# Performance work log

Measured on AMD Instinct MI355X. Metric: run time of the kernel, lower is better.

The kernel has to match this reference:

```python
import jax, jax.numpy as jnp
import numpy as np
from jax import lax


def _b3_kernel_2d(dtype=jnp.float32):
    k1 = jnp.array([1.0 / 16.0, 1.0 / 4.0, 3.0 / 8.0, 1.0 / 4.0, 1.0 / 16.0], dtype=dtype)
    return jnp.outer(k1, k1)  # (5, 5)


def _dilated_b3_conv(x, kernel_2d, dilation):
    # PyTorch Conv2d(kernel_size=5, dilation=d, padding=2*d, padding_mode='reflect')
    pad = 2 * dilation
    xp = jnp.pad(x, ((0, 0), (0, 0), (pad, pad), (pad, pad)), mode='reflect')
    k = kernel_2d[None, None, :, :]  # (O=1, I=1, 5, 5)
    return lax.conv_general_dilated(
        xp, k,
        window_strides=(1, 1),
        padding='VALID',
        rhs_dilation=(dilation, dilation),
        dimension_numbers=('NCHW', 'OIHW', 'NCHW'),
    )


def setup_inputs() -> dict:
    key = jax.random.key(0)
    B, H, W = 16, 1024, 1024
    x = jax.random.normal(key, (B, 1, H, W), dtype=jnp.float32)
    kernel_2d = _b3_kernel_2d(jnp.float32)
    return {"x": x, "kernel_2d": kernel_2d, "n_scales": 5}


def reference(x, kernel_2d, n_scales):
    # a trous starlet transform: detail_j = c_j - c_{j+1}; last channel = coarse
    detail_scales = []
    coarse = x
    for scale_idx in range(n_scales - 1):
        dilation = 2 ** scale_idx
        next_coarse = _dilated_b3_conv(coarse, kernel_2d, dilation)
        detail_scales.append(coarse - next_coarse)
        coarse = next_coarse
    all_scales = detail_scales + [coarse]
    return jnp.concatenate(all_scales, axis=1)  # (B, n_scales, H, W)
```

## Files before the change

### kernel.cpp

```cpp
#include <hip/hip_runtime.h>

#define TX 64
#define TY 64

template<int D>
__global__ __launch_bounds__(256)
void starlet_scale(const float* __restrict__ in, long in_bs,
                   float* __restrict__ det,      long det_bs,
                   float* __restrict__ coa,      long coa_bs)
{
    constexpr int H = 1024, W = 1024;
    constexpr int R  = 2 * D;
    constexpr int LW = TX + 2 * R;
    constexpr int LH = TY + 2 * R;
    constexpr int LS = LW + 1;

    __shared__ float tile[LH * LS];
    __shared__ float htmp[LH * TX];

    const int tid = threadIdx.x;
    const int bx  = blockIdx.x * TX;
    const int by  = blockIdx.y * TY;
    const int b   = blockIdx.z;

    const float* __restrict__ inp = in + (long)b * in_bs;

    const float k0 = 0.0625f;
    const float k1 = 0.25f;
    const float k2 = 0.375f;

    for (int i = tid; i < LH * LW; i += 256) {
        int ly = i / LW;
        int lx = i - ly * LW;
        int gy = by - R + ly;
        gy = (gy < 0) ? -gy : ((gy >= H) ? (2 * H - 2 - gy) : gy);
        int gx = bx - R + lx;
        gx = (gx < 0) ? -gx : ((gx >= W) ? (2 * W - 2 - gx) : gx);
        tile[ly * LS + lx] = inp[(long)gy * W + gx];
    }
    __syncthreads();

    for (int i = tid; i < LH * TX; i += 256) {
        int r = i >> 6;
        int x = i & (TX - 1);
        const float* t = &tile[r * LS + x];
        htmp[i] = k0 * (t[0] + t[4 * D]) + k1 * (t[D] + t[3 * D]) + k2 * t[2 * D];
    }
    __syncthreads();

    for (int i = tid; i < TY * TX; i += 256) {
        int y = i >> 6;
        int x = i & (TX - 1);
        const float* h = &htmp[y * TX + x];
        float conv = k0 * (h[0] + h[4 * D * TX])
                   + k1 * (h[D * TX] + h[3 * D * TX])
                   + k2 * h[2 * D * TX];
        float center = tile[(y + R) * LS + (x + R)];
        long gidx = (long)(by + y) * W + (bx + x);
        det[(long)b * det_bs + gidx] = center - conv;
        coa[(long)b * coa_bs + gidx] = conv;
    }
}

extern "C" void kernel_launch(void* const* d_in, const int* in_sizes, int n_in,
                              void* d_out, int out_size, void* d_ws, size_t ws_size,
                              hipStream_t stream) {
    const float* x = (const float*)d_in[0];
    float* out = (float*)d_out;
    float* ws  = (float*)d_ws;

    const long HW = 1024L * 1024L;
    const long OB = 5 * HW;

    dim3 grid(1024 / TX, 1024 / TY, 16);
    dim3 block(256);

    starlet_scale<1><<<grid, block, 0, stream>>>(x, HW, out + 0 * HW, OB, ws, HW);
    starlet_scale<2><<<grid, block, 0, stream>>>(ws, HW, out + 1 * HW, OB, out + 4 * HW, OB);
    starlet_scale<4><<<grid, block, 0, stream>>>(out + 4 * HW, OB, out + 2 * HW, OB, ws, HW);
    starlet_scale<8><<<grid, block, 0, stream>>>(ws, HW, out + 3 * HW, OB, out + 4 * HW, OB);
}
```

Baseline: 513.2 us.

## Fuse starlet scales pairwise into two kernels with float4 tiles and WG swizzle

```diff
diff --git a/kernel.cpp b/kernel.cpp
--- a/kernel.cpp
+++ b/kernel.cpp
@@ -1,64 +1,238 @@
 #include <hip/hip_runtime.h>
 
-#define TX 64
-#define TY 64
-
-template<int D>
-__global__ __launch_bounds__(256)
-void starlet_scale(const float* __restrict__ in, long in_bs,
-                   float* __restrict__ det,      long det_bs,
-                   float* __restrict__ coa,      long coa_bs)
+
+constexpr int H = 1024, W = 1024;
+constexpr long HW = (long)H * W;
+constexpr long OB = 5 * HW;
+constexpr int NT = 256;
+
+__device__ __forceinline__ int reflect_i(int g, int n) {
+    g = (g < 0) ? -g : g;
+    return (g >= n) ? (2 * n - 2 - g) : g;
+}
+
+__device__ __forceinline__ void swizzle_wg(int gx, int gy, int& tx, int& ty, int& tb) {
+    const int nwg = gx * gy * (int)gridDim.z;
+    const int lin = (int)blockIdx.x + gx * ((int)blockIdx.y + gy * (int)blockIdx.z);
+    const int work = (lin & 7) * (nwg >> 3) + (lin >> 3);
+    tx = work % gx;
+    const int rest = work / gx;
+    ty = rest % gy;
+    tb = rest / gy;
+}
+
+__device__ __forceinline__ float4 f4sub(float4 a, float4 b) {
+    return float4{a.x - b.x, a.y - b.y, a.z - b.z, a.w - b.w};
+}
+
+__global__ __launch_bounds__(256, 3)
+void starlet_s01(const float* __restrict__ in, float* __restrict__ out, float* __restrict__ ws)
 {
-    constexpr int H = 1024, W = 1024;
-    constexpr int R  = 2 * D;
-    constexpr int LW = TX + 2 * R;
-    constexpr int LH = TY + 2 * R;
-    constexpr int LS = LW + 1;
-
-    __shared__ float tile[LH * LS];
-    __shared__ float htmp[LH * TX];
-
+    constexpr int ROWS = 76, AV = 20, SA = 21, SB = 19;
+    __shared__ float4 A4[ROWS * SA];
+    __shared__ float4 B4[ROWS * SB];
+    const float k0 = 0.0625f, k1 = 0.25f, k2 = 0.375f;
+
+    int tx, ty, tb;
+    swizzle_wg(16, 16, tx, ty, tb);
+    const int bx = tx * 64, by = ty * 64;
     const int tid = threadIdx.x;
-    const int bx  = blockIdx.x * TX;
-    const int by  = blockIdx.y * TY;
-    const int b   = blockIdx.z;
-
-    const float* __restrict__ inp = in + (long)b * in_bs;
-
-    const float k0 = 0.0625f;
-    const float k1 = 0.25f;
-    const float k2 = 0.375f;
-
-    for (int i = tid; i < LH * LW; i += 256) {
-        int ly = i / LW;
-        int lx = i - ly * LW;
-        int gy = by - R + ly;
-        gy = (gy < 0) ? -gy : ((gy >= H) ? (2 * H - 2 - gy) : gy);
-        int gx = bx - R + lx;
-        gx = (gx < 0) ? -gx : ((gx >= W) ? (2 * W - 2 - gx) : gx);
-        tile[ly * LS + lx] = inp[(long)gy * W + gx];
-    }
-    __syncthreads();
-
-    for (int i = tid; i < LH * TX; i += 256) {
-        int r = i >> 6;
-        int x = i & (TX - 1);
-        const float* t = &tile[r * LS + x];
-        htmp[i] = k0 * (t[0] + t[4 * D]) + k1 * (t[D] + t[3 * D]) + k2 * t[2 * D];
-    }
-    __syncthreads();
-
-    for (int i = tid; i < TY * TX; i += 256) {
-        int y = i >> 6;
-        int x = i & (TX - 1);
-        const float* h = &htmp[y * TX + x];
-        float conv = k0 * (h[0] + h[4 * D * TX])
-                   + k1 * (h[D * TX] + h[3 * D * TX])
-                   + k2 * h[2 * D * TX];
-        float center = tile[(y + R) * LS + (x + R)];
-        long gidx = (long)(by + y) * W + (bx + x);
-        det[(long)b * det_bs + gidx] = center - conv;
-        coa[(long)b * coa_bs + gidx] = conv;
+    const float* __restrict__ inp = in + (long)tb * HW;
+
+    if (bx >= 8 && bx + 72 <= W && by >= 6 && by + 70 <= H) {
+        const float* src = inp + (long)(by - 6) * W + (bx - 8);
+        for (int t = tid; t < ROWS * AV; t += NT) {
+            int r = t / AV, c = t - r * AV;
+            A4[r * SA + c] = *(const float4*)(src + (long)r * W + 4 * c);
+        }
+    } else {
+        float* Af = (float*)A4;
+        for (int t = tid; t < ROWS * 4 * AV; t += NT) {
+            int r = t / (4 * AV), c = t - r * (4 * AV);
+            Af[r * (4 * SA) + c] = inp[(long)reflect_i(by - 6 + r, H) * W + reflect_i(bx - 8 + c, W)];
+        }
+    }
+    __syncthreads();
+
+    for (int t = tid; t < ROWS * 18; t += NT) {
+        int r = t / 18, h = t - r * 18;
+        float4 v0 = A4[r * SA + h], v1 = A4[r * SA + h + 1], v2 = A4[r * SA + h + 2];
+        float f[12] = {v0.x, v0.y, v0.z, v0.w, v1.x, v1.y, v1.z, v1.w, v2.x, v2.y, v2.z, v2.w};
+        float4 o;
+        o.x = k0 * (f[2] + f[6]) + k1 * (f[3] + f[5]) + k2 * f[4];
+        o.y = k0 * (f[3] + f[7]) + k1 * (f[4] + f[6]) + k2 * f[5];
+        o.z = k0 * (f[4] + f[8]) + k1 * (f[5] + f[7]) + k2 * f[6];
+        o.w = k0 * (f[5] + f[9]) + k1 * (f[6] + f[8]) + k2 * f[7];
+        B4[r * SB + h] = o;
+    }
+    __syncthreads();
+
+    {
+        float* det0 = out + (long)tb * OB;
+        for (int t = tid; t < 18 * 18; t += NT) {
+            int g = t / 18, h = t - g * 18;
+            float4 rr[8];
+            #pragma unroll
+            for (int m = 0; m < 8; ++m) rr[m] = B4[(4 * g + m) * SB + h];
+            #pragma unroll
+            for (int k = 0; k < 4; ++k) {
+                float4 c1;
+                c1.x = k0 * (rr[k].x + rr[k+4].x) + k1 * (rr[k+1].x + rr[k+3].x) + k2 * rr[k+2].x;
+                c1.y = k0 * (rr[k].y + rr[k+4].y) + k1 * (rr[k+1].y + rr[k+3].y) + k2 * rr[k+2].y;
+                c1.z = k0 * (rr[k].z + rr[k+4].z) + k1 * (rr[k+1].z + rr[k+3].z) + k2 * rr[k+2].z;
+                c1.w = k0 * (rr[k].w + rr[k+4].w) + k1 * (rr[k+1].w + rr[k+3].w) + k2 * rr[k+2].w;
+                const int y = 4 * g + k - 4;
+                const int slot = (y + 6) * SA + h + 1;
+                float4 old = A4[slot];
+                A4[slot] = c1;
+                if (y >= 0 && y < 64 && h >= 1 && h < 17)
+                    *(float4*)(det0 + (long)(by + y) * W + bx + 4 * h - 4) = f4sub(old, c1);
+            }
+        }
+    }
+    __syncthreads();
+
+    for (int t = tid; t < 72 * 16; t += NT) {
+        int r = t / 16, h1 = t - r * 16;
+        int base = (r + 2) * SA + h1 + 1;
+        float4 v0 = A4[base], v1 = A4[base + 1], v2 = A4[base + 2];
+        float f[12] = {v0.x, v0.y, v0.z, v0.w, v1.x, v1.y, v1.z, v1.w, v2.x, v2.y, v2.z, v2.w};
+        float4 o;
+        o.x = k0 * (f[0] + f[8])  + k1 * (f[2] + f[6])  + k2 * f[4];
+        o.y = k0 * (f[1] + f[9])  + k1 * (f[3] + f[7])  + k2 * f[5];
+        o.z = k0 * (f[2] + f[10]) + k1 * (f[4] + f[8])  + k2 * f[6];
+        o.w = k0 * (f[3] + f[11]) + k1 * (f[5] + f[9])  + k2 * f[7];
+        B4[(r + 2) * SB + h1] = o;
+    }
+    __syncthreads();
+
+    {
+        const int h1 = tid & 15, u = tid >> 4;
+        const int c = u & 1, g = u >> 1;
+        float4 rr[8];
+        #pragma unroll
+        for (int m = 0; m < 8; ++m) rr[m] = B4[(2 + c + 8 * g + 2 * m) * SB + h1];
+        float* det1 = out + (long)tb * OB + HW;
+        float* coa  = ws + (long)tb * HW;
+        #pragma unroll
+        for (int k = 0; k < 4; ++k) {
+            float4 c2;
+            c2.x = k0 * (rr[k].x + rr[k+4].x) + k1 * (rr[k+1].x + rr[k+3].x) + k2 * rr[k+2].x;
+            c2.y = k0 * (rr[k].y + rr[k+4].y) + k1 * (rr[k+1].y + rr[k+3].y) + k2 * rr[k+2].y;
+            c2.z = k0 * (rr[k].z + rr[k+4].z) + k1 * (rr[k+1].z + rr[k+3].z) + k2 * rr[k+2].z;
+            c2.w = k0 * (rr[k].w + rr[k+4].w) + k1 * (rr[k+1].w + rr[k+3].w) + k2 * rr[k+2].w;
+            const int y = c + 2 * (4 * g + k);
+            float4 old = A4[(y + 6) * SA + h1 + 2];
+            const long gofs = (long)(by + y) * W + bx + 4 * h1;
+            *(float4*)(det1 + gofs) = f4sub(old, c2);
+            *(float4*)(coa + gofs) = c2;
+        }
+    }
+}
+
+__global__ __launch_bounds__(256, 2)
+void starlet_s23(const float* __restrict__ in, float* __restrict__ out)
+{
+    constexpr int ROWS = 112, AV = 20, SA = 21, SB = 17;
+    __shared__ float4 A4[ROWS * SA];
+    __shared__ float4 B4[ROWS * SB];
+    const float k0 = 0.0625f, k1 = 0.25f, k2 = 0.375f;
+
+    int tx, ty, tb;
+    swizzle_wg(32, 16, tx, ty, tb);
+    const int bx = tx * 32, by = ty * 64;
+    const int tid = threadIdx.x;
+    const float* __restrict__ inp = in + (long)tb * HW;
+
+    if (bx >= 24 && bx + 56 <= W && by >= 24 && by + 88 <= H) {
+        const float* src = inp + (long)(by - 24) * W + (bx - 24);
+        for (int t = tid; t < ROWS * AV; t += NT) {
+            int r = t / AV, c = t - r * AV;
+            A4[r * SA + c] = *(const float4*)(src + (long)r * W + 4 * c);
+        }
+    } else {
+        float* Af = (float*)A4;
+        for (int t = tid; t < ROWS * 4 * AV; t += NT) {
+            int r = t / (4 * AV), c = t - r * (4 * AV);
+            Af[r * (4 * SA) + c] = inp[(long)reflect_i(by - 24 + r, H) * W + reflect_i(bx - 24 + c, W)];
+        }
+    }
+    __syncthreads();
+
+    for (int t = tid; t < ROWS * 16; t += NT) {
+        int r = t / 16, h = t - r * 16;
+        int base = r * SA + h;
+        float4 t0 = A4[base], t1 = A4[base + 1], t2 = A4[base + 2], t3 = A4[base + 3], t4 = A4[base + 4];
+        float4 o;
+        o.x = k0 * (t0.x + t4.x) + k1 * (t1.x + t3.x) + k2 * t2.x;
+        o.y = k0 * (t0.y + t4.y) + k1 * (t1.y + t3.y) + k2 * t2.y;
+        o.z = k0 * (t0.z + t4.z) + k1 * (t1.z + t3.z) + k2 * t2.z;
+        o.w = k0 * (t0.w + t4.w) + k1 * (t1.w + t3.w) + k2 * t2.w;
+        B4[r * SB + h] = o;
+    }
+    __syncthreads();
+
+    {
+        float* det2 = out + (long)tb * OB + 2 * HW;
+        for (int t = tid; t < 384; t += NT) {
+            int h = t & 15, u = t >> 4;
+            int c = u & 3, g = u >> 2;
+            float4 rr[8];
+            #pragma unroll
+            for (int m = 0; m < 8; ++m) rr[m] = B4[(c + 16 * g + 4 * m) * SB + h];
+            #pragma unroll
+            for (int k = 0; k < 4; ++k) {
+                float4 c3;
+                c3.x = k0 * (rr[k].x + rr[k+4].x) + k1 * (rr[k+1].x + rr[k+3].x) + k2 * rr[k+2].x;
+                c3.y = k0 * (rr[k].y + rr[k+4].y) + k1 * (rr[k+1].y + rr[k+3].y) + k2 * rr[k+2].y;
+                c3.z = k0 * (rr[k].z + rr[k+4].z) + k1 * (rr[k+1].z + rr[k+3].z) + k2 * rr[k+2].z;
+                c3.w = k0 * (rr[k].w + rr[k+4].w) + k1 * (rr[k+1].w + rr[k+3].w) + k2 * rr[k+2].w;
+                const int y = -16 + c + 4 * (4 * g + k);
+                const int slot = (y + 24) * SA + h + 2;
+                float4 old = A4[slot];
+                A4[slot] = c3;
+                if (y >= 0 && y < 64 && h >= 4 && h < 12)
+                    *(float4*)(det2 + (long)(by + y) * W + bx + 4 * h - 16) = f4sub(old, c3);
+            }
+        }
+    }
+    __syncthreads();
+
+    for (int t = tid; t < 96 * 8; t += NT) {
+        int r2 = t / 8, h3 = t - r2 * 8;
+        int arow = r2 + 8;
+        int base = arow * SA + h3;
+        float4 t0 = A4[base + 2], t1 = A4[base + 4], t2 = A4[base + 6], t3 = A4[base + 8], t4 = A4[base + 10];
+        float4 o;
+        o.x = k0 * (t0.x + t4.x) + k1 * (t1.x + t3.x) + k2 * t2.x;
+        o.y = k0 * (t0.y + t4.y) + k1 * (t1.y + t3.y) + k2 * t2.y;
+        o.z = k0 * (t0.z + t4.z) + k1 * (t1.z + t3.z) + k2 * t2.z;
+        o.w = k0 * (t0.w + t4.w) + k1 * (t1.w + t3.w) + k2 * t2.w;
+        B4[arow * SB + h3] = o;
+    }
+    __syncthreads();
+
+    if (tid < 128) {
+        const int h3 = tid & 7, u = tid >> 3;
+        const int c = u & 7, g = u >> 3;
+        float4 rr[8];
+        #pragma unroll
+        for (int m = 0; m < 8; ++m) rr[m] = B4[(8 + c + 32 * g + 8 * m) * SB + h3];
+        float* det3 = out + (long)tb * OB + 3 * HW;
+        float* coa4 = out + (long)tb * OB + 4 * HW;
+        #pragma unroll
+        for (int k = 0; k < 4; ++k) {
+            float4 c4;
+            c4.x = k0 * (rr[k].x + rr[k+4].x) + k1 * (rr[k+1].x + rr[k+3].x) + k2 * rr[k+2].x;
+            c4.y = k0 * (rr[k].y + rr[k+4].y) + k1 * (rr[k+1].y + rr[k+3].y) + k2 * rr[k+2].y;
+            c4.z = k0 * (rr[k].z + rr[k+4].z) + k1 * (rr[k+1].z + rr[k+3].z) + k2 * rr[k+2].z;
+            c4.w = k0 * (rr[k].w + rr[k+4].w) + k1 * (rr[k+1].w + rr[k+3].w) + k2 * rr[k+2].w;
+            const int y = c + 8 * (4 * g + k);
+            float4 old = A4[(y + 24) * SA + h3 + 6];
+            const long gofs = (long)(by + y) * W + bx + 4 * h3;
+            *(float4*)(det3 + gofs) = f4sub(old, c4);
+            *(float4*)(coa4 + gofs) = c4;
+        }
     }
 }
 
@@ -68,15 +242,9 @@
     const float* x = (const float*)d_in[0];
     float* out = (float*)d_out;
     float* ws  = (float*)d_ws;
-
-    const long HW = 1024L * 1024L;
-    const long OB = 5 * HW;
-
-    dim3 grid(1024 / TX, 1024 / TY, 16);
-    dim3 block(256);
-
-    starlet_scale<1><<<grid, block, 0, stream>>>(x, HW, out + 0 * HW, OB, ws, HW);
-    starlet_scale<2><<<grid, block, 0, stream>>>(ws, HW, out + 1 * HW, OB, out + 4 * HW, OB);
-    starlet_scale<4><<<grid, block, 0, stream>>>(out + 4 * HW, OB, out + 2 * HW, OB, ws, HW);
-    starlet_scale<8><<<grid, block, 0, stream>>>(ws, HW, out + 3 * HW, OB, out + 4 * HW, OB);
-}
+    (void)in_sizes; (void)n_in; (void)ws_size; (void)out_size;
+
+    dim3 gA(16, 16, 16), gB(32, 16, 16);
+    starlet_s01<<<gA, dim3(NT), 0, stream>>>(x, out, ws);
+    starlet_s23<<<gB, dim3(NT), 0, stream>>>(ws, out);
+}
```

After: 503.9 us. No clear change (-1.8%).
